# Kernel optimization log

Hardware: AMD Instinct MI355X
Metric: run time of the kernel (lower is better)

## Reference

```python
import jax, jax.numpy as jnp
import numpy as np

N_NODES = 100000
N_EDGES = 1600000
IN_FEAT = 64
OUT_FEAT = 64


def setup_inputs() -> dict:
    key = jax.random.key(0)
    k_feat, k_src, k_dst, k_tw, k_tb, k_pw, k_pb = jax.random.split(key, 7)
    bound = 1.0 / np.sqrt(IN_FEAT)
    return {
        "feat": jax.random.normal(k_feat, (N_NODES, IN_FEAT), dtype=jnp.float32),
        "src": jax.random.randint(k_src, (N_EDGES,), 0, N_NODES, dtype=jnp.int32),
        "dst": jax.random.randint(k_dst, (N_EDGES,), 0, N_NODES, dtype=jnp.int32),
        "theta_w": jax.random.uniform(k_tw, (OUT_FEAT, IN_FEAT), jnp.float32, -bound, bound),
        "theta_b": jax.random.uniform(k_tb, (OUT_FEAT,), jnp.float32, -bound, bound),
        "phi_w": jax.random.uniform(k_pw, (OUT_FEAT, IN_FEAT), jnp.float32, -bound, bound),
        "phi_b": jax.random.uniform(k_pb, (OUT_FEAT,), jnp.float32, -bound, bound),
    }


def reference(feat, src, dst, theta_w, theta_b, phi_w, phi_b):
    # Two dense projections: h_theta = theta(feat), h_phi = phi(feat)
    h_theta = feat @ theta_w.T + theta_b          # [N, out_feat]
    h_phi = feat @ phi_w.T + phi_b                # [N, out_feat]
    diff = h_phi - h_theta                        # dstdata['x']
    # u_add_v: per-edge message e = h_theta[src] + (h_phi - h_theta)[dst]
    e = h_theta[src] + diff[dst]                  # [E, out_feat]
    # fn.max('e', 'x'): segment max over destination nodes
    out = jax.ops.segment_max(e, dst, num_segments=N_NODES)  # [N, out_feat]
    # DGL fills zero-in-degree destinations with 0 (segment_max yields -inf)
    return jnp.where(jnp.isfinite(out), out, jnp.float32(0))
```

## Files before the change

### kernel.cpp

```cpp
#include <hip/hip_runtime.h>
#include <hip/hip_bf16.h>
#include <hip/hip_fp16.h>

#define F 64
#define BSH 7
#define NBMAX 1024
#define CHUNK 4096
#define EPT 8
#define BCAP 4096
#define WPAD 72

typedef __bf16 bf16x8 __attribute__((ext_vector_type(8)));
typedef float  f32x4  __attribute__((ext_vector_type(4)));
typedef unsigned int uint4v __attribute__((ext_vector_type(4)));

__device__ inline unsigned pkmax(unsigned a, unsigned b) {
    unsigned d;
    asm volatile("v_pk_max_f16 %0, %1, %2" : "=v"(d) : "v"(a), "v"(b));
    return d;
}
__device__ inline uint4v pkmax4(uint4v a, uint4v b) {
    uint4v r;
    r.x = pkmax(a.x, b.x); r.y = pkmax(a.y, b.y);
    r.z = pkmax(a.z, b.z); r.w = pkmax(a.w, b.w);
    return r;
}
__device__ inline float half_lo(unsigned u) {
    union { unsigned short s; _Float16 h; } c; c.s = (unsigned short)(u & 0xFFFF);
    return (float)c.h;
}
__device__ inline float half_hi(unsigned u) {
    union { unsigned short s; _Float16 h; } c; c.s = (unsigned short)(u >> 16);
    return (float)c.h;
}
__device__ inline void casmax(unsigned* a, unsigned val) {
    unsigned old = *a;
    while (true) {
        unsigned nw = pkmax(old, val);
        if (nw == old) break;
        unsigned prev = atomicCAS(a, old, nw);
        if (prev == old) break;
        old = prev;
    }
}

union FusedSh {
    struct { __bf16 w2t[128 * WPAD]; float bias[128]; } p;
    struct {
        int cur[NBMAX]; int gb[NBMAX]; int lbeg[NBMAX];
        int fs[512];
        unsigned sw[CHUNK];
        unsigned short sb[CHUNK];
    } b;
};

__global__ __launch_bounds__(512) void fused_proj_bin(
    const float* __restrict__ feat,
    const float* __restrict__ theta_w, const float* __restrict__ theta_b,
    const float* __restrict__ phi_w,  const float* __restrict__ phi_b,
    _Float16* __restrict__ h16, _Float16* __restrict__ d16,
    const int* __restrict__ src, const int* __restrict__ dst,
    int* __restrict__ bcnt, unsigned* __restrict__ packed,
    int n_nodes, int n_edges, int nb, int bin_blocks, int proj_blocks)
{
    __shared__ FusedSh sh;
    const int t = threadIdx.x;

    if (blockIdx.x < bin_blocks) {
        const int base = blockIdx.x * CHUNK;
        const int cnt = min(CHUNK, n_edges - base);

        for (int i = t; i < NBMAX; i += 512) sh.b.cur[i] = 0;
        __syncthreads();

        unsigned w[EPT];
        int      bk[EPT];
        int      rk[EPT];
        const int k0 = t * EPT;

        if (k0 + EPT <= cnt) {
            #pragma unroll
            for (int j = 0; j < EPT; ++j) {
                int k = k0 + j;
                int s = src[base + k], d = dst[base + k];
                w[j]  = ((unsigned)(d & ((1 << BSH) - 1)) << 17) | (unsigned)s;
                int b = d >> BSH;
                bk[j] = b;
                rk[j] = atomicAdd(&sh.b.cur[b], 1);
            }
        } else {
            #pragma unroll
            for (int j = 0; j < EPT; ++j) {
                int k = k0 + j;
                bk[j] = -1;
                if (k < cnt) {
                    int s = src[base + k], d = dst[base + k];
                    w[j]  = ((unsigned)(d & ((1 << BSH) - 1)) << 17) | (unsigned)s;
                    int b = d >> BSH;
                    bk[j] = b;
                    rk[j] = atomicAdd(&sh.b.cur[b], 1);
                }
            }
        }
        __syncthreads();

        for (int i = t; i < nb; i += 512) {
            int c = sh.b.cur[i];
            sh.b.gb[i] = c ? atomicAdd(&bcnt[i], c) : 0;
        }

        int c0 = sh.b.cur[2 * t];
        int c1 = sh.b.cur[2 * t + 1];
        int s2 = c0 + c1;
        sh.b.fs[t] = s2;
        __syncthreads();
        for (int off = 1; off < 512; off <<= 1) {
            int x = (t >= off) ? sh.b.fs[t - off] : 0;
            __syncthreads();
            sh.b.fs[t] += x;
            __syncthreads();
        }
        {
            int exc = sh.b.fs[t] - s2;
            sh.b.lbeg[2 * t]     = exc;
            sh.b.lbeg[2 * t + 1] = exc + c0;
        }
        __syncthreads();

        #pragma unroll
        for (int j = 0; j < EPT; ++j) {
            if (bk[j] >= 0) {
                int slot = sh.b.lbeg[bk[j]] + rk[j];
                sh.b.sw[slot] = w[j];
                sh.b.sb[slot] = (unsigned short)bk[j];
            }
        }
        __syncthreads();

        #pragma unroll
        for (int r = 0; r < EPT; ++r) {
            int p = r * 512 + t;
            if (p < cnt) {
                int b = sh.b.sb[p];
                int pos = sh.b.gb[b] + (p - sh.b.lbeg[b]);
                if (pos < BCAP) packed[(size_t)b * BCAP + pos] = sh.b.sw[p];
            }
        }
    } else {
        const int pb = blockIdx.x - bin_blocks;

        for (int i = t; i < 128 * 64; i += 512) {
            int n = i >> 6, k = i & 63;
            float v = (n < 64) ? theta_w[n * 64 + k]
                               : phi_w[(n - 64) * 64 + k] - theta_w[(n - 64) * 64 + k];
            sh.p.w2t[n * WPAD + k] = (__bf16)v;
        }
        if (t < 128) {
            int n = t;
            sh.p.bias[n] = (n < 64) ? theta_b[n] : (phi_b[n - 64] - theta_b[n - 64]);
        }
        __syncthreads();

        const int lane = t & 63;
        const int wv   = t >> 6;
        const int m    = lane & 15;
        const int q    = lane >> 4;
        const int nchunks = (n_nodes + 127) >> 7;

        for (int ch = pb; ch < nchunks; ch += proj_blocks) {
            const int rowbase = ch * 128 + wv * 16;
            int arow = rowbase + m;
            int rs = arow < n_nodes ? arow : 0;

            bf16x8 a0, a1;
            {
                const float* p0 = feat + (size_t)rs * 64 + q * 8;
                #pragma unroll
                for (int j = 0; j < 8; ++j) a0[j] = (__bf16)p0[j];
                #pragma unroll
                for (int j = 0; j < 8; ++j) a1[j] = (__bf16)p0[32 + j];
            }

            f32x4 acc[8];
            #pragma unroll
            for (int c = 0; c < 8; ++c) acc[c] = (f32x4){0.f, 0.f, 0.f, 0.f};

            #pragma unroll
            for (int c = 0; c < 8; ++c) {
                const __bf16* wp = &sh.p.w2t[(c * 16 + m) * WPAD + q * 8];
                bf16x8 b0 = *(const bf16x8*)wp;
                bf16x8 b1 = *(const bf16x8*)(wp + 32);
                acc[c] = __builtin_amdgcn_mfma_f32_16x16x32_bf16(a0, b0, acc[c], 0, 0, 0);
                acc[c] = __builtin_amdgcn_mfma_f32_16x16x32_bf16(a1, b1, acc[c], 0, 0, 0);
            }

            #pragma unroll
            for (int c = 0; c < 8; ++c) {
                float bb = sh.p.bias[c * 16 + m];
                #pragma unroll
                for (int r = 0; r < 4; ++r) {
                    int orow = rowbase + q * 4 + r;
                    if (orow < n_nodes) {
                        float v = acc[c][r] + bb;
                        if (c < 4)
                            h16[(size_t)orow * F + c * 16 + m] = (_Float16)v;
                        else
                            d16[(size_t)orow * F + (c - 4) * 16 + m] = (_Float16)v;
                    }
                }
            }
        }
    }
}

__global__ __launch_bounds__(256) void sort_reduce(
    const unsigned* __restrict__ packed, const int* __restrict__ bcnt,
    const _Float16* __restrict__ h16, const _Float16* __restrict__ d16,
    float* __restrict__ out, int n_nodes)
{
    __shared__ unsigned ew[BCAP];
    __shared__ unsigned mx[128 * 32];
    __shared__ int fcnt[128];
    __shared__ int fbg[129];
    __shared__ int fs[256];

    const int b = blockIdx.x, t = threadIdx.x;
    const int beg = b * BCAP;
    const int cnt = min(bcnt[b], BCAP);
    const unsigned NEGI = 0xFC00FC00u;

    #pragma unroll
    for (int i = 0; i < 16; ++i) mx[i * 256 + t] = NEGI;
    if (t < 128) fcnt[t] = 0;
    __syncthreads();

    unsigned w[16];
    int      rk[16];
    #pragma unroll
    for (int j = 0; j < 16; ++j) {
        int k = j * 256 + t;
        rk[j] = -1;
        if (k < cnt) {
            unsigned wrd = packed[beg + k];
            w[j]  = wrd;
            rk[j] = atomicAdd(&fcnt[wrd >> 17], 1);
        }
    }
    __syncthreads();

    int v = (t < 128) ? fcnt[t] : 0;
    fs[t] = v;
    __syncthreads();
    for (int off = 1; off < 128; off <<= 1) {
        int x = (t >= off) ? fs[t - off] : 0;
        __syncthreads();
        fs[t] += x;
        __syncthreads();
    }
    if (t < 128) fbg[t] = fs[t] - v;
    if (t == 0)  fbg[128] = cnt;
    __syncthreads();

    #pragma unroll
    for (int j = 0; j < 16; ++j) {
        if (rk[j] >= 0) {
            unsigned wrd = w[j];
            ew[fbg[wrd >> 17] + rk[j]] = wrd & 0x1FFFFu;
        }
    }
    __syncthreads();

    const int g  = t >> 3;
    const int f8 = t & 7;
    {
        int L0 = (cnt + 31) >> 5;
        int L  = ((L0 + 3) & ~7) | 4;
        int s  = g * L; if (s > cnt) s = cnt;
        int e  = s + L; if (e > cnt) e = cnt;

        if (s < e) {
            int lo = 0, hi = 128;
            while (lo + 1 < hi) {
                int mid = (lo + hi) >> 1;
                if (fbg[mid] <= s) lo = mid; else hi = mid;
            }
            int node = lo;
            int nend = fbg[node + 1];

            uint4v acc = (uint4v){NEGI, NEGI, NEGI, NEGI};
            int p = s;
            for (; p + 4 <= e; p += 4) {
                uint4v sv = *(const uint4v*)&ew[p];
                uint4v v0 = *(const uint4v*)(h16 + (size_t)sv.x * F + f8 * 8);
                uint4v v1 = *(const uint4v*)(h16 + (size_t)sv.y * F + f8 * 8);
                uint4v v2 = *(const uint4v*)(h16 + (size_t)sv.z * F + f8 * 8);
                uint4v v3 = *(const uint4v*)(h16 + (size_t)sv.w * F + f8 * 8);
                while (p >= nend) {
                    unsigned* m0 = &mx[node * 32 + f8 * 4];
                    casmax(m0 + 0, acc.x); casmax(m0 + 1, acc.y);
                    casmax(m0 + 2, acc.z); casmax(m0 + 3, acc.w);
                    acc = (uint4v){NEGI, NEGI, NEGI, NEGI};
                    ++node; nend = fbg[node + 1];
                }
                acc = pkmax4(acc, v0);
                while (p + 1 >= nend) {
                    unsigned* m0 = &mx[node * 32 + f8 * 4];
                    casmax(m0 + 0, acc.x); casmax(m0 + 1, acc.y);
                    casmax(m0 + 2, acc.z); casmax(m0 + 3, acc.w);
                    acc = (uint4v){NEGI, NEGI, NEGI, NEGI};
                    ++node; nend = fbg[node + 1];
                }
                acc = pkmax4(acc, v1);
                while (p + 2 >= nend) {
                    unsigned* m0 = &mx[node * 32 + f8 * 4];
                    casmax(m0 + 0, acc.x); casmax(m0 + 1, acc.y);
                    casmax(m0 + 2, acc.z); casmax(m0 + 3, acc.w);
                    acc = (uint4v){NEGI, NEGI, NEGI, NEGI};
                    ++node; nend = fbg[node + 1];
                }
                acc = pkmax4(acc, v2);
                while (p + 3 >= nend) {
                    unsigned* m0 = &mx[node * 32 + f8 * 4];
                    casmax(m0 + 0, acc.x); casmax(m0 + 1, acc.y);
                    casmax(m0 + 2, acc.z); casmax(m0 + 3, acc.w);
                    acc = (uint4v){NEGI, NEGI, NEGI, NEGI};
                    ++node; nend = fbg[node + 1];
                }
                acc = pkmax4(acc, v3);
            }
            for (; p < e; ++p) {
                unsigned srcn = ew[p];
                uint4v v0 = *(const uint4v*)(h16 + (size_t)srcn * F + f8 * 8);
                while (p >= nend) {
                    unsigned* m0 = &mx[node * 32 + f8 * 4];
                    casmax(m0 + 0, acc.x); casmax(m0 + 1, acc.y);
                    casmax(m0 + 2, acc.z); casmax(m0 + 3, acc.w);
                    acc = (uint4v){NEGI, NEGI, NEGI, NEGI};
                    ++node; nend = fbg[node + 1];
                }
                acc = pkmax4(acc, v0);
            }
            unsigned* m0 = &mx[node * 32 + f8 * 4];
            casmax(m0 + 0, acc.x); casmax(m0 + 1, acc.y);
            casmax(m0 + 2, acc.z); casmax(m0 + 3, acc.w);
        }
    }
    __syncthreads();

    const int ln0 = t >> 3;
    #pragma unroll
    for (int pass = 0; pass < 4; ++pass) {
        int ln = ln0 + pass * 32;
        int node = (b << BSH) + ln;
        if (node < n_nodes) {
            size_t o = (size_t)node * F + f8 * 8;
            f32x4 r0, r1;
            if (fcnt[ln] > 0) {
                uint4v A  = *(const uint4v*)&mx[ln * 32 + f8 * 4];
                uint4v dv = __builtin_nontemporal_load((const uint4v*)(d16 + o));
                r0[0] = half_lo(dv.x) + half_lo(A.x);
                r0[1] = half_hi(dv.x) + half_hi(A.x);
                r0[2] = half_lo(dv.y) + half_lo(A.y);
                r0[3] = half_hi(dv.y) + half_hi(A.y);
                r1[0] = half_lo(dv.z) + half_lo(A.z);
                r1[1] = half_hi(dv.z) + half_hi(A.z);
                r1[2] = half_lo(dv.w) + half_lo(A.w);
                r1[3] = half_hi(dv.w) + half_hi(A.w);
            } else {
                r0 = (f32x4){0.f, 0.f, 0.f, 0.f};
                r1 = (f32x4){0.f, 0.f, 0.f, 0.f};
            }
            __builtin_nontemporal_store(r0, (f32x4*)(out + o));
            __builtin_nontemporal_store(r1, (f32x4*)(out + o + 4));
        }
    }
}

extern "C" void kernel_launch(void* const* d_in, const int* in_sizes, int n_in,
                              void* d_out, int out_size, void* d_ws, size_t ws_size,
                              hipStream_t stream) {
    const float* feat    = (const float*)d_in[0];
    const int*   src     = (const int*)d_in[1];
    const int*   dst     = (const int*)d_in[2];
    const float* theta_w = (const float*)d_in[3];
    const float* theta_b = (const float*)d_in[4];
    const float* phi_w   = (const float*)d_in[5];
    const float* phi_b   = (const float*)d_in[6];
    float* out = (float*)d_out;

    const int n_nodes = in_sizes[0] / F;
    const int n_edges = in_sizes[1];
    const int nb      = (n_nodes + (1 << BSH) - 1) >> BSH;

    _Float16* h16    = (_Float16*)d_ws;
    _Float16* d16    = h16 + (size_t)n_nodes * F;
    unsigned* packed = (unsigned*)(d16 + (size_t)n_nodes * F);
    int*      bcnt   = (int*)(packed + (size_t)nb * BCAP);

    hipMemsetAsync(bcnt, 0, NBMAX * sizeof(int), stream);

    const int bin_blocks  = (n_edges + CHUNK - 1) / CHUNK;
    const int proj_blocks = 391;
    fused_proj_bin<<<bin_blocks + proj_blocks, 512, 0, stream>>>(
        feat, theta_w, theta_b, phi_w, phi_b, h16, d16,
        src, dst, bcnt, packed, n_nodes, n_edges, nb, bin_blocks, proj_blocks);

    sort_reduce<<<nb, 256, 0, stream>>>(packed, bcnt, h16, d16, out, n_nodes);
}
```

Measured before the change: 150.0 us.

## Stage projection outputs in LDS for coalesced 16-byte stores, one chunk per block

Projection results are now written to a padded shared-memory staging tile and then copied out as 16-byte vector stores per row, replacing scattered 2-byte global stores. The persistent grid-stride loop over chunks is dropped; each projection block handles exactly one 128-row chunk and the grid grows to cover all nodes. This is meant to cut global store transaction count, at the cost of extra syncs, shared-memory traffic and re-staging the weights in every block.

```diff
diff --git a/kernel.cpp b/kernel.cpp
--- a/kernel.cpp
+++ b/kernel.cpp
@@ -9,6 +9,7 @@
 #define EPT 8
 #define BCAP 4096
 #define WPAD 72
+#define SPAD 136
 
 typedef __bf16 bf16x8 __attribute__((ext_vector_type(8)));
 typedef float  f32x4  __attribute__((ext_vector_type(4)));
@@ -45,7 +46,13 @@
 }
 
 union FusedSh {
-    struct { __bf16 w2t[128 * WPAD]; float bias[128]; } p;
+    struct {
+        union {
+            __bf16  w2t[128 * WPAD];
+            _Float16 stage[128 * SPAD];
+        } u;
+        float bias[128];
+    } p;
     struct {
         int cur[NBMAX]; int gb[NBMAX]; int lbeg[NBMAX];
         int fs[512];
@@ -61,7 +68,7 @@
     _Float16* __restrict__ h16, _Float16* __restrict__ d16,
     const int* __restrict__ src, const int* __restrict__ dst,
     int* __restrict__ bcnt, unsigned* __restrict__ packed,
-    int n_nodes, int n_edges, int nb, int bin_blocks, int proj_blocks)
+    int n_nodes, int n_edges, int nb, int bin_blocks)
 {
     __shared__ FusedSh sh;
     const int t = threadIdx.x;
@@ -148,12 +155,13 @@
         }
     } else {
         const int pb = blockIdx.x - bin_blocks;
+        const int chunkbase = pb * 128;
 
         for (int i = t; i < 128 * 64; i += 512) {
             int n = i >> 6, k = i & 63;
             float v = (n < 64) ? theta_w[n * 64 + k]
                                : phi_w[(n - 64) * 64 + k] - theta_w[(n - 64) * 64 + k];
-            sh.p.w2t[n * WPAD + k] = (__bf16)v;
+            sh.p.u.w2t[n * WPAD + k] = (__bf16)v;
         }
         if (t < 128) {
             int n = t;
@@ -165,49 +173,56 @@
         const int wv   = t >> 6;
         const int m    = lane & 15;
         const int q    = lane >> 4;
-        const int nchunks = (n_nodes + 127) >> 7;
-
-        for (int ch = pb; ch < nchunks; ch += proj_blocks) {
-            const int rowbase = ch * 128 + wv * 16;
-            int arow = rowbase + m;
-            int rs = arow < n_nodes ? arow : 0;
-
-            bf16x8 a0, a1;
-            {
-                const float* p0 = feat + (size_t)rs * 64 + q * 8;
-                #pragma unroll
-                for (int j = 0; j < 8; ++j) a0[j] = (__bf16)p0[j];
-                #pragma unroll
-                for (int j = 0; j < 8; ++j) a1[j] = (__bf16)p0[32 + j];
-            }
-
-            f32x4 acc[8];
+
+        const int rowbase = chunkbase + wv * 16;
+        int arow = rowbase + m;
+        int rs = arow < n_nodes ? arow : 0;
+
+        bf16x8 a0, a1;
+        {
+            const float* p0 = feat + (size_t)rs * 64 + q * 8;
             #pragma unroll
-            for (int c = 0; c < 8; ++c) acc[c] = (f32x4){0.f, 0.f, 0.f, 0.f};
-
+            for (int j = 0; j < 8; ++j) a0[j] = (__bf16)p0[j];
             #pragma unroll
-            for (int c = 0; c < 8; ++c) {
-                const __bf16* wp = &sh.p.w2t[(c * 16 + m) * WPAD + q * 8];
-                bf16x8 b0 = *(const bf16x8*)wp;
-                bf16x8 b1 = *(const bf16x8*)(wp + 32);
-                acc[c] = __builtin_amdgcn_mfma_f32_16x16x32_bf16(a0, b0, acc[c], 0, 0, 0);
-                acc[c] = __builtin_amdgcn_mfma_f32_16x16x32_bf16(a1, b1, acc[c], 0, 0, 0);
-            }
-
+            for (int j = 0; j < 8; ++j) a1[j] = (__bf16)p0[32 + j];
+        }
+
+        f32x4 acc[8];
+        #pragma unroll
+        for (int c = 0; c < 8; ++c) acc[c] = (f32x4){0.f, 0.f, 0.f, 0.f};
+
+        #pragma unroll
+        for (int c = 0; c < 8; ++c) {
+            const __bf16* wp = &sh.p.u.w2t[(c * 16 + m) * WPAD + q * 8];
+            bf16x8 b0 = *(const bf16x8*)wp;
+            bf16x8 b1 = *(const bf16x8*)(wp + 32);
+            acc[c] = __builtin_amdgcn_mfma_f32_16x16x32_bf16(a0, b0, acc[c], 0, 0, 0);
+            acc[c] = __builtin_amdgcn_mfma_f32_16x16x32_bf16(a1, b1, acc[c], 0, 0, 0);
+        }
+
+        __syncthreads();
+
+        const int rloc = wv * 16 + q * 4;
+        #pragma unroll
+        for (int c = 0; c < 8; ++c) {
+            float bb = sh.p.bias[c * 16 + m];
             #pragma unroll
-            for (int c = 0; c < 8; ++c) {
-                float bb = sh.p.bias[c * 16 + m];
-                #pragma unroll
-                for (int r = 0; r < 4; ++r) {
-                    int orow = rowbase + q * 4 + r;
-                    if (orow < n_nodes) {
-                        float v = acc[c][r] + bb;
-                        if (c < 4)
-                            h16[(size_t)orow * F + c * 16 + m] = (_Float16)v;
-                        else
-                            d16[(size_t)orow * F + (c - 4) * 16 + m] = (_Float16)v;
-                    }
-                }
+            for (int r = 0; r < 4; ++r)
+                sh.p.u.stage[(rloc + r) * SPAD + c * 16 + m] =
+                    (_Float16)(acc[c][r] + bb);
+        }
+        __syncthreads();
+
+        #pragma unroll
+        for (int p2 = 0; p2 < 2; ++p2) {
+            int idx = p2 * 512 + t;
+            int row = idx >> 3, c8 = idx & 7;
+            int grow = chunkbase + row;
+            if (grow < n_nodes) {
+                uint4v hv = *(const uint4v*)&sh.p.u.stage[row * SPAD + c8 * 8];
+                uint4v dv = *(const uint4v*)&sh.p.u.stage[row * SPAD + 64 + c8 * 8];
+                *(uint4v*)(h16 + (size_t)grow * F + c8 * 8) = hv;
+                *(uint4v*)(d16 + (size_t)grow * F + c8 * 8) = dv;
             }
         }
     }
@@ -400,10 +415,10 @@
     hipMemsetAsync(bcnt, 0, NBMAX * sizeof(int), stream);
 
     const int bin_blocks  = (n_edges + CHUNK - 1) / CHUNK;
-    const int proj_blocks = 391;
+    const int proj_blocks = (n_nodes + 127) / 128;
     fused_proj_bin<<<bin_blocks + proj_blocks, 512, 0, stream>>>(
         feat, theta_w, theta_b, phi_w, phi_b, h16, d16,
-        src, dst, bcnt, packed, n_nodes, n_edges, nb, bin_blocks, proj_blocks);
+        src, dst, bcnt, packed, n_nodes, n_edges, nb, bin_blocks);
 
     sort_reduce<<<nb, 256, 0, stream>>>(packed, bcnt, h16, d16, out, n_nodes);
 }
```

After: 147.8 us. No clear change (-1.5%).
